# Kernel tuning notes

Hardware: AMD Instinct MI355X
Metric: run time of the kernel (lower is better)

## Reference

```python
import jax, jax.numpy as jnp
import numpy as np

NV, NQ, K, C, FF, H = 40000, 8192, 96, 128, 256, 8
DH = C // H


def _layernorm(x, g, b, eps=1e-5):
    m = jnp.mean(x, axis=-1, keepdims=True)
    v = jnp.var(x, axis=-1, keepdims=True)
    return (x - m) * jax.lax.rsqrt(v + eps) * g + b


def setup_inputs() -> dict:
    key = jax.random.key(0)
    ks = jax.random.split(key, 20)
    voxel_features = jax.random.normal(ks[0], (NV, C), dtype=jnp.float32)
    voxel_coords = jax.random.normal(ks[1], (NV, 3), dtype=jnp.float32)
    query_coords = jax.random.normal(ks[2], (NQ, 3), dtype=jnp.float32)
    raw = jax.random.randint(ks[3], (NQ, K), 0, 50000)
    key_indices = jnp.where(raw >= NV, -1, raw)  # -1 marks padded/missing keys
    key_indices = key_indices.at[:, 0].set(raw[:, 0] % NV)  # ensure >=1 valid key per query
    w = lambda k, shape: (jax.random.normal(k, shape, dtype=jnp.float32) * 0.02)
    return {
        "voxel_features": voxel_features,
        "voxel_coords": voxel_coords,
        "query_coords": query_coords,
        "key_indices": key_indices,
        "norm1_g": jnp.ones((C,), jnp.float32), "norm1_b": jnp.zeros((C,), jnp.float32),
        "q_pos_w": w(ks[4], (C, 3)), "q_pos_b": jnp.zeros((C,), jnp.float32),
        "k_pos_w": w(ks[5], (C, 3)), "k_pos_b": jnp.zeros((C,), jnp.float32),
        "in_w": w(ks[6], (3 * C, C)), "in_b": jnp.zeros((3 * C,), jnp.float32),
        "out_w": w(ks[7], (C, C)), "out_b": jnp.zeros((C,), jnp.float32),
        "norm2_g": jnp.ones((C,), jnp.float32), "norm2_b": jnp.zeros((C,), jnp.float32),
        "lin1_w": w(ks[8], (FF, C)), "lin1_b": jnp.zeros((FF,), jnp.float32),
        "lin2_w": w(ks[9], (C, FF)), "lin2_b": jnp.zeros((C,), jnp.float32),
        "fin_w": w(ks[10], (C, C)), "fin_b": jnp.zeros((C,), jnp.float32),
    }


def reference(voxel_features, voxel_coords, query_coords, key_indices,
              norm1_g, norm1_b, q_pos_w, q_pos_b, k_pos_w, k_pos_b,
              in_w, in_b, out_w, out_b, norm2_g, norm2_b,
              lin1_w, lin1_b, lin2_w, lin2_b, fin_w, fin_b):
    mask = key_indices < 0                      # [NQ, K] True = padded
    idx = jnp.where(mask, 0, key_indices)
    vf = _layernorm(voxel_features, norm1_g, norm1_b)   # norm1
    key_feat = vf[idx]                          # gather: [NQ, K, C]
    key_c = voxel_coords[idx]                   # [NQ, K, 3]
    # q_pos_proj: Linear(3,C)+ReLU ; k_pos_proj: Conv1d(3,C,1)+ReLU (== per-key linear)
    q_feat = jax.nn.relu(query_coords @ q_pos_w.T + q_pos_b)        # [NQ, C]
    key_pos = jax.nn.relu(jnp.einsum('nkt,ct->nkc', key_c, k_pos_w) + k_pos_b)
    key_feat = key_feat + key_pos               # [NQ, K, C]
    # nn.MultiheadAttention: query [1,NQ,C], key/value [K,NQ,C] -> per-query attention over K keys
    wq, wk, wv = in_w[:C], in_w[C:2 * C], in_w[2 * C:]
    bq, bk, bv = in_b[:C], in_b[C:2 * C], in_b[2 * C:]
    q = (q_feat @ wq.T + bq).reshape(NQ, H, DH)                 # [NQ,H,DH]
    k = (key_feat @ wk.T + bk).reshape(NQ, K, H, DH)            # [NQ,K,H,DH]
    v = (key_feat @ wv.T + bv).reshape(NQ, K, H, DH)
    scale = 1.0 / np.sqrt(DH)
    scores = jnp.einsum('nhd,nkhd->nhk', q, k) * scale          # [NQ,H,K]
    scores = jnp.where(mask[:, None, :], jnp.float32(-1e9), scores)
    attn = jax.nn.softmax(scores, axis=-1)
    ctx = jnp.einsum('nhk,nkhd->nhd', attn, v).reshape(NQ, C)
    attend = ctx @ out_w.T + out_b                              # [NQ,C]
    # FFN block (dropout=0 -> identity)
    h = _layernorm(attend, norm2_g, norm2_b)
    act = jax.nn.relu(h @ lin1_w.T + lin1_b) @ lin2_w.T + lin2_b
    x = attend + act
    out = jax.nn.relu(x @ fin_w.T + fin_b)                      # output_layer
    return out
```

## Files before the change

kernel.cpp:

```cpp
#include <hip/hip_runtime.h>
#include <hip/hip_bf16.h>
#include <math.h>

constexpr int NVOX = 40000;
constexpr int NQRY = 8192;
constexpr int KK   = 96;
constexpr int CH   = 128;
constexpr int FFD  = 256;

typedef __attribute__((ext_vector_type(8))) short short8;
typedef __attribute__((ext_vector_type(4))) float float4v;

__device__ inline float bflo(unsigned u) { return __uint_as_float(u << 16); }
__device__ inline float bfhi(unsigned u) { return __uint_as_float(u & 0xffff0000u); }
__device__ inline unsigned short f2bf(float x) {
  union { float f; unsigned u; } a; a.f = x;
  const unsigned r = a.u + 0x7fffu + ((a.u >> 16) & 1u);
  return (unsigned short)(r >> 16);
}
__device__ inline unsigned pack2(float lo, float hi) {
  return (unsigned)f2bf(lo) | ((unsigned)f2bf(hi) << 16);
}

__global__ __launch_bounds__(256) void k_prep(
    const float* __restrict__ vfeat, const float* __restrict__ vcoord,
    const float* __restrict__ n1g, const float* __restrict__ n1b,
    const float* __restrict__ kpw, const float* __restrict__ kpb,
    const float* __restrict__ in_w,
    const float* __restrict__ ow, const float* __restrict__ l1w,
    const float* __restrict__ l2w, const float* __restrict__ fw,
    __hip_bfloat16* __restrict__ Gb, __hip_bfloat16* __restrict__ Wb,
    __hip_bfloat16* __restrict__ Eb) {
  const int b = blockIdx.x;
  const int t = threadIdx.x;
  if (b < NVOX/16) {
    const int vloc = t >> 4;
    const int l    = t & 15;
    const int j = b * 16 + vloc;
    const float4* vrow = reinterpret_cast<const float4*>(vfeat + (size_t)j * CH);
    const float4 x0 = vrow[l*2], x1 = vrow[l*2+1];
    float s  = x0.x+x0.y+x0.z+x0.w + x1.x+x1.y+x1.z+x1.w;
    float ss = x0.x*x0.x+x0.y*x0.y+x0.z*x0.z+x0.w*x0.w
             + x1.x*x1.x+x1.y*x1.y+x1.z*x1.z+x1.w*x1.w;
    #pragma unroll
    for (int m = 8; m >= 1; m >>= 1) { s += __shfl_xor(s, m); ss += __shfl_xor(ss, m); }
    const float mean = s * (1.0f/CH);
    const float var  = ss * (1.0f/CH) - mean*mean;
    const float rstd = 1.0f / sqrtf(var + 1e-5f);
    const float c0 = vcoord[j*3+0], c1 = vcoord[j*3+1], c2 = vcoord[j*3+2];
    const float xv[8] = {x0.x,x0.y,x0.z,x0.w,x1.x,x1.y,x1.z,x1.w};
    float gv[8];
    #pragma unroll
    for (int u = 0; u < 8; u++) {
      const int c = l*8 + u;
      const float vf = (xv[u] - mean) * rstd * n1g[c] + n1b[c];
      const float kp = fmaf(c0, kpw[c*3+0], fmaf(c1, kpw[c*3+1], fmaf(c2, kpw[c*3+2], kpb[c])));
      gv[u] = vf + fmaxf(kp, 0.0f);
    }
    const uint4 pk = make_uint4(pack2(gv[0],gv[1]), pack2(gv[2],gv[3]),
                                pack2(gv[4],gv[5]), pack2(gv[6],gv[7]));
    *reinterpret_cast<uint4*>(Gb + (size_t)j*CH + l*8) = pk;
  } else {
    const int idx = b - NVOX/16;
    const float* src;
    __hip_bfloat16* dst;
    if (idx < 8) {
      const int e = (idx * 256 + t) * 16;
      src = in_w + (size_t)CH*CH + e;
      dst = Wb + e;
    } else {
      const int f = ((idx - 8) * 256 + t) * 16;
      dst = Eb + f;
      if      (f < 16384) src = ow  + f;
      else if (f < 49152) src = l1w + (f - 16384);
      else if (f < 81920) src = l2w + (f - 49152);
      else                src = fw  + (f - 81920);
    }
    float v[16];
    #pragma unroll
    for (int u = 0; u < 4; u++) {
      const float4 fq = *reinterpret_cast<const float4*>(src + u*4);
      v[u*4+0]=fq.x; v[u*4+1]=fq.y; v[u*4+2]=fq.z; v[u*4+3]=fq.w;
    }
    uint4* o = reinterpret_cast<uint4*>(dst);
    o[0] = make_uint4(pack2(v[0],v[1]), pack2(v[2],v[3]),
                      pack2(v[4],v[5]), pack2(v[6],v[7]));
    o[1] = make_uint4(pack2(v[8],v[9]), pack2(v[10],v[11]),
                      pack2(v[12],v[13]), pack2(v[14],v[15]));
  }
}

__global__ __launch_bounds__(256) void k_kv_gemm(
    const __hip_bfloat16* __restrict__ Gb, const __hip_bfloat16* __restrict__ Wb,
    const float* __restrict__ in_b,
    unsigned short* __restrict__ KVh) {
  __shared__ unsigned short ldsD[64][72];
  const int t = threadIdx.x;
  const int w = t >> 6;
  const int lane = t & 63;
  const int col = lane & 15;
  const int quad = lane >> 4;
  const int bx = blockIdx.x;
  const int v0 = (bx >> 2) * 64;
  const int cg = bx & 3;

  const unsigned short* gRow =
      reinterpret_cast<const unsigned short*>(Gb) + (size_t)(v0 + w*16 + col)*CH + quad*8;
  short8 afrag[4];
  #pragma unroll
  for (int kq = 0; kq < 4; kq++)
    afrag[kq] = *reinterpret_cast<const short8*>(gRow + kq*32);

  float4v acc[4];
  #pragma unroll
  for (int j = 0; j < 4; j++) {
    const float bia = in_b[CH + cg*64 + j*16 + col];
    acc[j] = (float4v){bia, bia, bia, bia};
  }
  const unsigned short* wB = reinterpret_cast<const unsigned short*>(Wb);
  #pragma unroll
  for (int kq = 0; kq < 4; kq++) {
    #pragma unroll
    for (int j = 0; j < 4; j++) {
      const short8 bfrag = *reinterpret_cast<const short8*>(
          wB + (size_t)(cg*64 + j*16 + col)*CH + kq*32 + quad*8);
      acc[j] = __builtin_amdgcn_mfma_f32_16x16x32_bf16(afrag[kq], bfrag, acc[j], 0, 0, 0);
    }
  }
  #pragma unroll
  for (int j = 0; j < 4; j++)
    #pragma unroll
    for (int r = 0; r < 4; r++)
      ldsD[w*16 + quad*4 + r][j*16 + col] = f2bf(acc[j][r]);
  __syncthreads();
  const int row = t >> 2;
  const int cc  = (t & 3) * 16;
  const uint4 d0 = *reinterpret_cast<const uint4*>(&ldsD[row][cc]);
  const uint4 d1 = *reinterpret_cast<const uint4*>(&ldsD[row][cc+8]);
  const int head = (cg & 1) * 4 + (cc >> 4);
  const int isV  = cg >> 1;
  unsigned short* dst = KVh + ((size_t)head*NVOX + (v0 + row))*32 + isV*16;
  uint4* out = reinterpret_cast<uint4*>(dst);
  out[0] = d0; out[1] = d1;
}

__global__ __launch_bounds__(256) void k_query(
    const float* __restrict__ qcoord,
    const float* __restrict__ qpw, const float* __restrict__ qpb,
    const float* __restrict__ in_w, const float* __restrict__ in_b,
    float* __restrict__ qout) {
  __shared__ float qf[16][CH];
  const int t = threadIdx.x;
  const int qbase = blockIdx.x * 16;
  #pragma unroll
  for (int i = 0; i < 8; i++) {
    const int e = t + 256*i;
    const int qv = e >> 7, c = e & 127;
    const int qq = qbase + qv;
    const float v = fmaf(qcoord[qq*3+0], qpw[c*3+0],
                    fmaf(qcoord[qq*3+1], qpw[c*3+1],
                    fmaf(qcoord[qq*3+2], qpw[c*3+2], qpb[c])));
    qf[qv][c] = fmaxf(v, 0.0f);
  }
  __syncthreads();
  const int oc = t & 127, half = t >> 7;
  const float* wrow = in_w + (size_t)oc * CH;
  const float bia = in_b[oc];
  float acc[8];
  #pragma unroll
  for (int v = 0; v < 8; v++) acc[v] = bia;
  for (int c = 0; c < CH; c += 4) {
    const float4 w4 = *reinterpret_cast<const float4*>(wrow + c);
    #pragma unroll
    for (int v = 0; v < 8; v++) {
      const float4 g4 = *reinterpret_cast<const float4*>(&qf[half*8+v][c]);
      acc[v] = fmaf(g4.x, w4.x, fmaf(g4.y, w4.y, fmaf(g4.z, w4.z, fmaf(g4.w, w4.w, acc[v]))));
    }
  }
  #pragma unroll
  for (int v = 0; v < 8; v++) qout[(size_t)(qbase + half*8 + v)*CH + oc] = acc[v];
}

__global__ __launch_bounds__(256) void k_attn(
    const unsigned short* __restrict__ KVh,
    const float* __restrict__ qg, const int* __restrict__ kidx,
    float* __restrict__ ctxg) {
  __shared__ float qs[8][16];
  __shared__ float sc[8*104];
  __shared__ float red[128][9];
  __shared__ float rden[8];
  const int t    = threadIdx.x;
  const int h    = blockIdx.x & 7;
  const int n0   = (blockIdx.x >> 3) * 8;
  const int w    = t >> 6;
  const int lane = t & 63;
  const int quad = lane >> 2;
  const int r    = lane & 3;
  const int qh   = quad >> 3;
  const int g    = quad & 7;
  const int q_l  = 2*w + qh;
  const unsigned short* KVbase = KVh + (size_t)h * NVOX * 32;

  if (t < 128) {
    const int q = t >> 4, d = t & 15;
    qs[q][d] = qg[(size_t)(n0 + q)*CH + h*16 + d];
  }
  unsigned msk = 0;
  uint4 kvbuf[12];
  const int krow = (n0 + q_l)*KK + g;
  #pragma unroll
  for (int it = 0; it < 12; it++) {
    const int j0 = kidx[krow + it*8];
    msk |= (unsigned)(j0 < 0) << it;
    const int j = (j0 < 0) ? 0 : j0;
    kvbuf[it] = *reinterpret_cast<const uint4*>(KVbase + (size_t)j*32 + r*8);
  }
  __syncthreads();
  const float4 qa = *reinterpret_cast<const float4*>(&qs[q_l][(r & 1)*8]);
  const float4 qb = *reinterpret_cast<const float4*>(&qs[q_l][(r & 1)*8 + 4]);
  #pragma unroll
  for (int it = 0; it < 12; it++) {
    const uint4 kv = kvbuf[it];
    float s = 0.0f;
    s = fmaf(qa.x, bflo(kv.x), s); s = fmaf(qa.y, bfhi(kv.x), s);
    s = fmaf(qa.z, bflo(kv.y), s); s = fmaf(qa.w, bfhi(kv.y), s);
    s = fmaf(qb.x, bflo(kv.z), s); s = fmaf(qb.y, bfhi(kv.z), s);
    s = fmaf(qb.z, bflo(kv.w), s); s = fmaf(qb.w, bfhi(kv.w), s);
    s += __shfl_xor(s, 1);
    if (r == 0)
      sc[q_l*104 + g + it*8] = ((msk >> it) & 1) ? -1e9f : s * 0.25f;
  }
  __syncthreads();
  if (t < 128) {
    const int q = t >> 4, l = t & 15;
    float mx = -3e38f;
    #pragma unroll
    for (int k = l; k < KK; k += 16) mx = fmaxf(mx, sc[q*104 + k]);
    #pragma unroll
    for (int m = 8; m >= 1; m >>= 1) mx = fmaxf(mx, __shfl_xor(mx, m));
    float sum = 0.0f;
    #pragma unroll
    for (int k = l; k < KK; k += 16) {
      const float p = __expf(sc[q*104 + k] - mx);
      sc[q*104 + k] = p;
      sum += p;
    }
    #pragma unroll
    for (int m = 8; m >= 1; m >>= 1) sum += __shfl_xor(sum, m);
    if (l == 0) rden[q] = 1.0f / sum;
  }
  __syncthreads();
  {
    float acc[8] = {0,0,0,0,0,0,0,0};
    #pragma unroll
    for (int it = 0; it < 12; it++) {
      const float wg = sc[q_l*104 + g + it*8];
      const uint4 kv = kvbuf[it];
      acc[0] = fmaf(wg, bflo(kv.x), acc[0]); acc[1] = fmaf(wg, bfhi(kv.x), acc[1]);
      acc[2] = fmaf(wg, bflo(kv.y), acc[2]); acc[3] = fmaf(wg, bfhi(kv.y), acc[3]);
      acc[4] = fmaf(wg, bflo(kv.z), acc[4]); acc[5] = fmaf(wg, bfhi(kv.z), acc[5]);
      acc[6] = fmaf(wg, bflo(kv.w), acc[6]); acc[7] = fmaf(wg, bfhi(kv.w), acc[7]);
    }
    if (r >= 2) {
      const int slot = q_l*16 + g*2 + (r - 2);
      #pragma unroll
      for (int u = 0; u < 8; u++) red[slot][u] = acc[u];
    }
  }
  __syncthreads();
  if (t < 128) {
    const int q = t >> 4, d = t & 15;
    const int half = d >> 3, u = d & 7;
    float s = 0.0f;
    #pragma unroll
    for (int gg = 0; gg < 8; gg++) s += red[q*16 + gg*2 + half][u];
    ctxg[(size_t)(n0 + q)*CH + h*16 + d] = s * rden[q];
  }
}

__global__ __launch_bounds__(256) void k_epi(
    const float* __restrict__ ctxg, const __hip_bfloat16* __restrict__ Eb,
    const float* __restrict__ ob,
    const float* __restrict__ n2g, const float* __restrict__ n2b,
    const float* __restrict__ l1b, const float* __restrict__ l2b,
    const float* __restrict__ fb,
    float* __restrict__ outp) {
  __shared__ unsigned short csb[16][136];
  __shared__ float attnS[16][132];
  __shared__ unsigned short hb[16][136];
  __shared__ unsigned short a1b[16][264];
  __shared__ unsigned short xb[16][136];
  const unsigned short* owb  = reinterpret_cast<const unsigned short*>(Eb);
  const unsigned short* l1wb = owb + 16384;
  const unsigned short* l2wb = owb + 49152;
  const unsigned short* fwb  = owb + 81920;

  const int t = threadIdx.x;
  const int w = t >> 6;
  const int lane = t & 63;
  const int col = lane & 15;
  const int quad = lane >> 4;
  const int qbase = blockIdx.x * 16;

  {
    const int e = t * 8;
    const int row = e >> 7, cc = e & 127;
    const float4* src = reinterpret_cast<const float4*>(ctxg + (size_t)(qbase+row)*CH + cc);
    const float4 x0 = src[0], x1 = src[1];
    *reinterpret_cast<uint4*>(&csb[row][cc]) =
        make_uint4(pack2(x0.x,x0.y), pack2(x0.z,x0.w), pack2(x1.x,x1.y), pack2(x1.z,x1.w));
  }
  __syncthreads();
  {
    short8 af[4];
    #pragma unroll
    for (int kq = 0; kq < 4; kq++)
      af[kq] = *reinterpret_cast<const short8*>(&csb[col][quad*8 + kq*32]);
    #pragma unroll
    for (int j = 0; j < 2; j++) {
      const int n0 = w*32 + j*16;
      const float bia = ob[n0 + col];
      float4v acc = (float4v){bia, bia, bia, bia};
      #pragma unroll
      for (int kq = 0; kq < 4; kq++) {
        const short8 bf = *reinterpret_cast<const short8*>(
            owb + (size_t)(n0 + col)*CH + kq*32 + quad*8);
        acc = __builtin_amdgcn_mfma_f32_16x16x32_bf16(af[kq], bf, acc, 0, 0, 0);
      }
      #pragma unroll
      for (int r = 0; r < 4; r++) attnS[quad*4 + r][n0 + col] = acc[r];
    }
  }
  __syncthreads();
  {
    const int row = t >> 4, l = t & 15;
    float s = 0.0f, ss = 0.0f;
    #pragma unroll
    for (int c = l; c < CH; c += 16) { const float x = attnS[row][c]; s += x; ss += x*x; }
    #pragma unroll
    for (int m = 8; m >= 1; m >>= 1) { s += __shfl_xor(s, m); ss += __shfl_xor(ss, m); }
    const float mean = s * (1.0f/CH);
    const float var  = ss * (1.0f/CH) - mean*mean;
    const float rstd = 1.0f / sqrtf(var + 1e-5f);
    #pragma unroll
    for (int c = l; c < CH; c += 16)
      hb[row][c] = f2bf((attnS[row][c] - mean) * rstd * n2g[c] + n2b[c]);
  }
  __syncthreads();
  {
    short8 af[4];
    #pragma unroll
    for (int kq = 0; kq < 4; kq++)
      af[kq] = *reinterpret_cast<const short8*>(&hb[col][quad*8 + kq*32]);
    #pragma unroll
    for (int j = 0; j < 4; j++) {
      const int n0 = w*64 + j*16;
      const float bia = l1b[n0 + col];
      float4v acc = (float4v){bia, bia, bia, bia};
      #pragma unroll
      for (int kq = 0; kq < 4; kq++) {
        const short8 bf = *reinterpret_cast<const short8*>(
            l1wb + (size_t)(n0 + col)*CH + kq*32 + quad*8);
        acc = __builtin_amdgcn_mfma_f32_16x16x32_bf16(af[kq], bf, acc, 0, 0, 0);
      }
      #pragma unroll
      for (int r = 0; r < 4; r++)
        a1b[quad*4 + r][n0 + col] = f2bf(fmaxf(acc[r], 0.0f));
    }
  }
  __syncthreads();
  {
    short8 af[8];
    #pragma unroll
    for (int kq = 0; kq < 8; kq++)
      af[kq] = *reinterpret_cast<const short8*>(&a1b[col][quad*8 + kq*32]);
    #pragma unroll
    for (int j = 0; j < 2; j++) {
      const int n0 = w*32 + j*16;
      const float bia = l2b[n0 + col];
      float4v acc = (float4v){bia, bia, bia, bia};
      #pragma unroll
      for (int kq = 0; kq < 8; kq++) {
        const short8 bf = *reinterpret_cast<const short8*>(
            l2wb + (size_t)(n0 + col)*FFD + kq*32 + quad*8);
        acc = __builtin_amdgcn_mfma_f32_16x16x32_bf16(af[kq], bf, acc, 0, 0, 0);
      }
      #pragma unroll
      for (int r = 0; r < 4; r++)
        xb[quad*4 + r][n0 + col] = f2bf(acc[r] + attnS[quad*4 + r][n0 + col]);
    }
  }
  __syncthreads();
  {
    short8 af[4];
    #pragma unroll
    for (int kq = 0; kq < 4; kq++)
      af[kq] = *reinterpret_cast<const short8*>(&xb[col][quad*8 + kq*32]);
    #pragma unroll
    for (int j = 0; j < 2; j++) {
      const int n0 = w*32 + j*16;
      const float bia = fb[n0 + col];
      float4v acc = (float4v){bia, bia, bia, bia};
      #pragma unroll
      for (int kq = 0; kq < 4; kq++) {
        const short8 bf = *reinterpret_cast<const short8*>(
            fwb + (size_t)(n0 + col)*CH + kq*32 + quad*8);
        acc = __builtin_amdgcn_mfma_f32_16x16x32_bf16(af[kq], bf, acc, 0, 0, 0);
      }
      #pragma unroll
      for (int r = 0; r < 4; r++)
        outp[(size_t)(qbase + quad*4 + r)*CH + n0 + col] = fmaxf(acc[r], 0.0f);
    }
  }
}

extern "C" void kernel_launch(void* const* d_in, const int* in_sizes, int n_in,
                              void* d_out, int out_size, void* d_ws, size_t ws_size,
                              hipStream_t stream) {
  const float* vfeat  = (const float*)d_in[0];
  const float* vcoord = (const float*)d_in[1];
  const float* qcoord = (const float*)d_in[2];
  const int*   kidx   = (const int*)  d_in[3];
  const float* n1g    = (const float*)d_in[4];
  const float* n1b    = (const float*)d_in[5];
  const float* qpw    = (const float*)d_in[6];
  const float* qpb    = (const float*)d_in[7];
  const float* kpw    = (const float*)d_in[8];
  const float* kpb    = (const float*)d_in[9];
  const float* in_w   = (const float*)d_in[10];
  const float* in_b   = (const float*)d_in[11];
  const float* out_w  = (const float*)d_in[12];
  const float* out_b  = (const float*)d_in[13];
  const float* n2g    = (const float*)d_in[14];
  const float* n2b    = (const float*)d_in[15];
  const float* l1w    = (const float*)d_in[16];
  const float* l1b    = (const float*)d_in[17];
  const float* l2w    = (const float*)d_in[18];
  const float* l2b    = (const float*)d_in[19];
  const float* fw     = (const float*)d_in[20];
  const float* fb     = (const float*)d_in[21];
  float* out = (float*)d_out;

  unsigned short* KVh = (unsigned short*)d_ws;
  __hip_bfloat16* Gb = (__hip_bfloat16*)(KVh + (size_t)8*NVOX*32);
  __hip_bfloat16* Wb = Gb + (size_t)NVOX*CH;
  __hip_bfloat16* Eb = Wb + (size_t)2*CH*CH;
  float* qb = (float*)(Eb + 98304);
  float* cx = qb + (size_t)NQRY*CH;

  k_prep   <<<NVOX/16 + 32, 256, 0, stream>>>(vfeat, vcoord, n1g, n1b, kpw, kpb,
                                              in_w, out_w, l1w, l2w, fw, Gb, Wb, Eb);
  k_query  <<<NQRY/16, 256, 0, stream>>>(qcoord, qpw, qpb, in_w, in_b, qb);
  k_kv_gemm<<<(NVOX/64)*4, 256, 0, stream>>>(Gb, Wb, in_b, KVh);
  k_attn   <<<(NQRY/8)*8, 256, 0, stream>>>(KVh, qb, kidx, cx);
  k_epi    <<<NQRY/16, 256, 0, stream>>>(cx, Eb, out_b, n2g, n2b, l1b, l2b, fb, out);
}
```

Baseline: 209.6 us.

## Fold query projection into prep kernel and make attention softmax register-resident

The query projection kernel becomes extra blocks of the prep kernel, which removes one launch and lets the two independent jobs share the GPU. The attention kernel now keeps scores in registers. Softmax max and sum are done with cross-lane shuffles, and the context reduction uses shuffles too, replacing shared-memory staging and four block-wide barriers. The cost is more shuffle traffic and a larger per-thread register array, and the prep kernel's shared-memory footprint grows for all of its blocks.

New measurement: 216.7 us. +3.4%, slower.

```diff
diff --git a/kernel.cpp b/kernel.cpp
--- a/kernel.cpp
+++ b/kernel.cpp
@@ -26,11 +26,13 @@
     const float* __restrict__ vfeat, const float* __restrict__ vcoord,
     const float* __restrict__ n1g, const float* __restrict__ n1b,
     const float* __restrict__ kpw, const float* __restrict__ kpb,
-    const float* __restrict__ in_w,
+    const float* __restrict__ in_w, const float* __restrict__ in_b,
     const float* __restrict__ ow, const float* __restrict__ l1w,
     const float* __restrict__ l2w, const float* __restrict__ fw,
+    const float* __restrict__ qcoord,
+    const float* __restrict__ qpw, const float* __restrict__ qpb,
     __hip_bfloat16* __restrict__ Gb, __hip_bfloat16* __restrict__ Wb,
-    __hip_bfloat16* __restrict__ Eb) {
+    __hip_bfloat16* __restrict__ Eb, float* __restrict__ qout) {
   const int b = blockIdx.x;
   const int t = threadIdx.x;
   if (b < NVOX/16) {
@@ -60,7 +62,7 @@
     const uint4 pk = make_uint4(pack2(gv[0],gv[1]), pack2(gv[2],gv[3]),
                                 pack2(gv[4],gv[5]), pack2(gv[6],gv[7]));
     *reinterpret_cast<uint4*>(Gb + (size_t)j*CH + l*8) = pk;
-  } else {
+  } else if (b < NVOX/16 + 32) {
     const int idx = b - NVOX/16;
     const float* src;
     __hip_bfloat16* dst;
@@ -87,6 +89,36 @@
                       pack2(v[4],v[5]), pack2(v[6],v[7]));
     o[1] = make_uint4(pack2(v[8],v[9]), pack2(v[10],v[11]),
                       pack2(v[12],v[13]), pack2(v[14],v[15]));
+  } else {
+    __shared__ float qf[16][CH];
+    const int qbase = (b - (NVOX/16 + 32)) * 16;
+    #pragma unroll
+    for (int i = 0; i < 8; i++) {
+      const int e = t + 256*i;
+      const int qv = e >> 7, c = e & 127;
+      const int qq = qbase + qv;
+      const float v = fmaf(qcoord[qq*3+0], qpw[c*3+0],
+                      fmaf(qcoord[qq*3+1], qpw[c*3+1],
+                      fmaf(qcoord[qq*3+2], qpw[c*3+2], qpb[c])));
+      qf[qv][c] = fmaxf(v, 0.0f);
+    }
+    __syncthreads();
+    const int oc = t & 127, half = t >> 7;
+    const float* wrow = in_w + (size_t)oc * CH;
+    const float bia = in_b[oc];
+    float acc[8];
+    #pragma unroll
+    for (int v = 0; v < 8; v++) acc[v] = bia;
+    for (int c = 0; c < CH; c += 4) {
+      const float4 w4 = *reinterpret_cast<const float4*>(wrow + c);
+      #pragma unroll
+      for (int v = 0; v < 8; v++) {
+        const float4 g4 = *reinterpret_cast<const float4*>(&qf[half*8+v][c]);
+        acc[v] = fmaf(g4.x, w4.x, fmaf(g4.y, w4.y, fmaf(g4.z, w4.z, fmaf(g4.w, w4.w, acc[v]))));
+      }
+    }
+    #pragma unroll
+    for (int v = 0; v < 8; v++) qout[(size_t)(qbase + half*8 + v)*CH + oc] = acc[v];
   }
 }
 
@@ -144,70 +176,28 @@
   out[0] = d0; out[1] = d1;
 }
 
-__global__ __launch_bounds__(256) void k_query(
-    const float* __restrict__ qcoord,
-    const float* __restrict__ qpw, const float* __restrict__ qpb,
-    const float* __restrict__ in_w, const float* __restrict__ in_b,
-    float* __restrict__ qout) {
-  __shared__ float qf[16][CH];
-  const int t = threadIdx.x;
-  const int qbase = blockIdx.x * 16;
-  #pragma unroll
-  for (int i = 0; i < 8; i++) {
-    const int e = t + 256*i;
-    const int qv = e >> 7, c = e & 127;
-    const int qq = qbase + qv;
-    const float v = fmaf(qcoord[qq*3+0], qpw[c*3+0],
-                    fmaf(qcoord[qq*3+1], qpw[c*3+1],
-                    fmaf(qcoord[qq*3+2], qpw[c*3+2], qpb[c])));
-    qf[qv][c] = fmaxf(v, 0.0f);
-  }
-  __syncthreads();
-  const int oc = t & 127, half = t >> 7;
-  const float* wrow = in_w + (size_t)oc * CH;
-  const float bia = in_b[oc];
-  float acc[8];
-  #pragma unroll
-  for (int v = 0; v < 8; v++) acc[v] = bia;
-  for (int c = 0; c < CH; c += 4) {
-    const float4 w4 = *reinterpret_cast<const float4*>(wrow + c);
-    #pragma unroll
-    for (int v = 0; v < 8; v++) {
-      const float4 g4 = *reinterpret_cast<const float4*>(&qf[half*8+v][c]);
-      acc[v] = fmaf(g4.x, w4.x, fmaf(g4.y, w4.y, fmaf(g4.z, w4.z, fmaf(g4.w, w4.w, acc[v]))));
-    }
-  }
-  #pragma unroll
-  for (int v = 0; v < 8; v++) qout[(size_t)(qbase + half*8 + v)*CH + oc] = acc[v];
-}
-
 __global__ __launch_bounds__(256) void k_attn(
     const unsigned short* __restrict__ KVh,
     const float* __restrict__ qg, const int* __restrict__ kidx,
     float* __restrict__ ctxg) {
-  __shared__ float qs[8][16];
-  __shared__ float sc[8*104];
-  __shared__ float red[128][9];
-  __shared__ float rden[8];
   const int t    = threadIdx.x;
   const int h    = blockIdx.x & 7;
   const int n0   = (blockIdx.x >> 3) * 8;
   const int w    = t >> 6;
   const int lane = t & 63;
-  const int quad = lane >> 2;
+  const int qh   = lane >> 5;
+  const int g    = (lane >> 2) & 7;
   const int r    = lane & 3;
-  const int qh   = quad >> 3;
-  const int g    = quad & 7;
-  const int q_l  = 2*w + qh;
+  const int q    = n0 + 2*w + qh;
   const unsigned short* KVbase = KVh + (size_t)h * NVOX * 32;
 
-  if (t < 128) {
-    const int q = t >> 4, d = t & 15;
-    qs[q][d] = qg[(size_t)(n0 + q)*CH + h*16 + d];
-  }
+  const float* qrow = qg + (size_t)q*CH + h*16 + (r & 1)*8;
+  const float4 qa = *reinterpret_cast<const float4*>(qrow);
+  const float4 qb = *reinterpret_cast<const float4*>(qrow + 4);
+
   unsigned msk = 0;
   uint4 kvbuf[12];
-  const int krow = (n0 + q_l)*KK + g;
+  const int krow = q*KK + g;
   #pragma unroll
   for (int it = 0; it < 12; it++) {
     const int j0 = kidx[krow + it*8];
@@ -215,9 +205,7 @@
     const int j = (j0 < 0) ? 0 : j0;
     kvbuf[it] = *reinterpret_cast<const uint4*>(KVbase + (size_t)j*32 + r*8);
   }
-  __syncthreads();
-  const float4 qa = *reinterpret_cast<const float4*>(&qs[q_l][(r & 1)*8]);
-  const float4 qb = *reinterpret_cast<const float4*>(&qs[q_l][(r & 1)*8 + 4]);
+  float sv[12];
   #pragma unroll
   for (int it = 0; it < 12; it++) {
     const uint4 kv = kvbuf[it];
@@ -227,54 +215,44 @@
     s = fmaf(qb.x, bflo(kv.z), s); s = fmaf(qb.y, bfhi(kv.z), s);
     s = fmaf(qb.z, bflo(kv.w), s); s = fmaf(qb.w, bfhi(kv.w), s);
     s += __shfl_xor(s, 1);
-    if (r == 0)
-      sc[q_l*104 + g + it*8] = ((msk >> it) & 1) ? -1e9f : s * 0.25f;
-  }
-  __syncthreads();
-  if (t < 128) {
-    const int q = t >> 4, l = t & 15;
-    float mx = -3e38f;
-    #pragma unroll
-    for (int k = l; k < KK; k += 16) mx = fmaxf(mx, sc[q*104 + k]);
-    #pragma unroll
-    for (int m = 8; m >= 1; m >>= 1) mx = fmaxf(mx, __shfl_xor(mx, m));
-    float sum = 0.0f;
-    #pragma unroll
-    for (int k = l; k < KK; k += 16) {
-      const float p = __expf(sc[q*104 + k] - mx);
-      sc[q*104 + k] = p;
-      sum += p;
-    }
-    #pragma unroll
-    for (int m = 8; m >= 1; m >>= 1) sum += __shfl_xor(sum, m);
-    if (l == 0) rden[q] = 1.0f / sum;
-  }
-  __syncthreads();
-  {
-    float acc[8] = {0,0,0,0,0,0,0,0};
-    #pragma unroll
-    for (int it = 0; it < 12; it++) {
-      const float wg = sc[q_l*104 + g + it*8];
-      const uint4 kv = kvbuf[it];
-      acc[0] = fmaf(wg, bflo(kv.x), acc[0]); acc[1] = fmaf(wg, bfhi(kv.x), acc[1]);
-      acc[2] = fmaf(wg, bflo(kv.y), acc[2]); acc[3] = fmaf(wg, bfhi(kv.y), acc[3]);
-      acc[4] = fmaf(wg, bflo(kv.z), acc[4]); acc[5] = fmaf(wg, bfhi(kv.z), acc[5]);
-      acc[6] = fmaf(wg, bflo(kv.w), acc[6]); acc[7] = fmaf(wg, bfhi(kv.w), acc[7]);
-    }
-    if (r >= 2) {
-      const int slot = q_l*16 + g*2 + (r - 2);
-      #pragma unroll
-      for (int u = 0; u < 8; u++) red[slot][u] = acc[u];
-    }
-  }
-  __syncthreads();
-  if (t < 128) {
-    const int q = t >> 4, d = t & 15;
-    const int half = d >> 3, u = d & 7;
-    float s = 0.0f;
-    #pragma unroll
-    for (int gg = 0; gg < 8; gg++) s += red[q*16 + gg*2 + half][u];
-    ctxg[(size_t)(n0 + q)*CH + h*16 + d] = s * rden[q];
+    sv[it] = ((msk >> it) & 1) ? -1e9f : s * 0.25f;
+  }
+  float mx = sv[0];
+  #pragma unroll
+  for (int it = 1; it < 12; it++) mx = fmaxf(mx, sv[it]);
+  mx = fmaxf(mx, __shfl_xor(mx, 4));
+  mx = fmaxf(mx, __shfl_xor(mx, 8));
+  mx = fmaxf(mx, __shfl_xor(mx, 16));
+  float sum = 0.0f;
+  #pragma unroll
+  for (int it = 0; it < 12; it++) { sv[it] = __expf(sv[it] - mx); sum += sv[it]; }
+  sum += __shfl_xor(sum, 4);
+  sum += __shfl_xor(sum, 8);
+  sum += __shfl_xor(sum, 16);
+  const float inv = 1.0f / sum;
+  const int qlane = lane & ~3;
+  #pragma unroll
+  for (int it = 0; it < 12; it++) sv[it] = __shfl(sv[it] * inv, qlane);
+  float acc[8] = {0,0,0,0,0,0,0,0};
+  #pragma unroll
+  for (int it = 0; it < 12; it++) {
+    const float wg = sv[it];
+    const uint4 kv = kvbuf[it];
+    acc[0] = fmaf(wg, bflo(kv.x), acc[0]); acc[1] = fmaf(wg, bfhi(kv.x), acc[1]);
+    acc[2] = fmaf(wg, bflo(kv.y), acc[2]); acc[3] = fmaf(wg, bfhi(kv.y), acc[3]);
+    acc[4] = fmaf(wg, bflo(kv.z), acc[4]); acc[5] = fmaf(wg, bfhi(kv.z), acc[5]);
+    acc[6] = fmaf(wg, bflo(kv.w), acc[6]); acc[7] = fmaf(wg, bfhi(kv.w), acc[7]);
+  }
+  #pragma unroll
+  for (int u = 0; u < 8; u++) {
+    acc[u] += __shfl_xor(acc[u], 4);
+    acc[u] += __shfl_xor(acc[u], 8);
+    acc[u] += __shfl_xor(acc[u], 16);
+  }
+  if (r >= 2 && g == 0) {
+    float* dst = ctxg + (size_t)q*CH + h*16 + (r - 2)*8;
+    *reinterpret_cast<float4*>(dst)     = make_float4(acc[0], acc[1], acc[2], acc[3]);
+    *reinterpret_cast<float4*>(dst + 4) = make_float4(acc[4], acc[5], acc[6], acc[7]);
   }
 }
 
@@ -448,9 +426,9 @@
   float* qb = (float*)(Eb + 98304);
   float* cx = qb + (size_t)NQRY*CH;
 
-  k_prep   <<<NVOX/16 + 32, 256, 0, stream>>>(vfeat, vcoord, n1g, n1b, kpw, kpb,
-                                              in_w, out_w, l1w, l2w, fw, Gb, Wb, Eb);
-  k_query  <<<NQRY/16, 256, 0, stream>>>(qcoord, qpw, qpb, in_w, in_b, qb);
+  k_prep   <<<NVOX/16 + 32 + NQRY/16, 256, 0, stream>>>(
+      vfeat, vcoord, n1g, n1b, kpw, kpb, in_w, in_b,
+      out_w, l1w, l2w, fw, qcoord, qpw, qpb, Gb, Wb, Eb, qb);
   k_kv_gemm<<<(NVOX/64)*4, 256, 0, stream>>>(Gb, Wb, in_b, KVh);
   k_attn   <<<(NQRY/8)*8, 256, 0, stream>>>(KVh, qb, kidx, cx);
   k_epi    <<<NQRY/16, 256, 0, stream>>>(cx, Eb, out_b, n2g, n2b, l1b, l2b, fb, out);
```

## Fold query projection into prep kernel and add cache-warming pass before attention

Applied to the files above, without the earlier changes.

Merges the query projection kernel into the prep kernel as extra blocks, saving one launch and letting that work overlap voxel normalization. Adds a k_warm kernel that reads the whole K/V table, the key indices and the query buffer right before attention, aiming to leave them in the last-level cache so the attention gathers hit in cache. The warm pass adds an extra full read of these buffers and one more launch, which only pays off if they stay resident in cache.

Result: no change. 211.2 us (+0.8%).

```diff
diff --git a/kernel.cpp b/kernel.cpp
--- a/kernel.cpp
+++ b/kernel.cpp
@@ -26,11 +26,13 @@
     const float* __restrict__ vfeat, const float* __restrict__ vcoord,
     const float* __restrict__ n1g, const float* __restrict__ n1b,
     const float* __restrict__ kpw, const float* __restrict__ kpb,
-    const float* __restrict__ in_w,
+    const float* __restrict__ in_w, const float* __restrict__ in_b,
     const float* __restrict__ ow, const float* __restrict__ l1w,
     const float* __restrict__ l2w, const float* __restrict__ fw,
+    const float* __restrict__ qcoord,
+    const float* __restrict__ qpw, const float* __restrict__ qpb,
     __hip_bfloat16* __restrict__ Gb, __hip_bfloat16* __restrict__ Wb,
-    __hip_bfloat16* __restrict__ Eb) {
+    __hip_bfloat16* __restrict__ Eb, float* __restrict__ qout) {
   const int b = blockIdx.x;
   const int t = threadIdx.x;
   if (b < NVOX/16) {
@@ -60,7 +62,7 @@
     const uint4 pk = make_uint4(pack2(gv[0],gv[1]), pack2(gv[2],gv[3]),
                                 pack2(gv[4],gv[5]), pack2(gv[6],gv[7]));
     *reinterpret_cast<uint4*>(Gb + (size_t)j*CH + l*8) = pk;
-  } else {
+  } else if (b < NVOX/16 + 32) {
     const int idx = b - NVOX/16;
     const float* src;
     __hip_bfloat16* dst;
@@ -87,6 +89,36 @@
                       pack2(v[4],v[5]), pack2(v[6],v[7]));
     o[1] = make_uint4(pack2(v[8],v[9]), pack2(v[10],v[11]),
                       pack2(v[12],v[13]), pack2(v[14],v[15]));
+  } else {
+    __shared__ float qf[16][CH];
+    const int qbase = (b - (NVOX/16 + 32)) * 16;
+    #pragma unroll
+    for (int i = 0; i < 8; i++) {
+      const int e = t + 256*i;
+      const int qv = e >> 7, c = e & 127;
+      const int qq = qbase + qv;
+      const float v = fmaf(qcoord[qq*3+0], qpw[c*3+0],
+                      fmaf(qcoord[qq*3+1], qpw[c*3+1],
+                      fmaf(qcoord[qq*3+2], qpw[c*3+2], qpb[c])));
+      qf[qv][c] = fmaxf(v, 0.0f);
+    }
+    __syncthreads();
+    const int oc = t & 127, half = t >> 7;
+    const float* wrow = in_w + (size_t)oc * CH;
+    const float bia = in_b[oc];
+    float acc[8];
+    #pragma unroll
+    for (int v = 0; v < 8; v++) acc[v] = bia;
+    for (int c = 0; c < CH; c += 4) {
+      const float4 w4 = *reinterpret_cast<const float4*>(wrow + c);
+      #pragma unroll
+      for (int v = 0; v < 8; v++) {
+        const float4 g4 = *reinterpret_cast<const float4*>(&qf[half*8+v][c]);
+        acc[v] = fmaf(g4.x, w4.x, fmaf(g4.y, w4.y, fmaf(g4.z, w4.z, fmaf(g4.w, w4.w, acc[v]))));
+      }
+    }
+    #pragma unroll
+    for (int v = 0; v < 8; v++) qout[(size_t)(qbase + half*8 + v)*CH + oc] = acc[v];
   }
 }
 
@@ -144,41 +176,30 @@
   out[0] = d0; out[1] = d1;
 }
 
-__global__ __launch_bounds__(256) void k_query(
-    const float* __restrict__ qcoord,
-    const float* __restrict__ qpw, const float* __restrict__ qpb,
-    const float* __restrict__ in_w, const float* __restrict__ in_b,
-    float* __restrict__ qout) {
-  __shared__ float qf[16][CH];
+__global__ __launch_bounds__(256) void k_warm(
+    const uint4* __restrict__ kv4, const uint4* __restrict__ kidx4,
+    const uint4* __restrict__ qg4, unsigned* __restrict__ sink) {
+  const int b = blockIdx.x;
   const int t = threadIdx.x;
-  const int qbase = blockIdx.x * 16;
-  #pragma unroll
-  for (int i = 0; i < 8; i++) {
-    const int e = t + 256*i;
-    const int qv = e >> 7, c = e & 127;
-    const int qq = qbase + qv;
-    const float v = fmaf(qcoord[qq*3+0], qpw[c*3+0],
-                    fmaf(qcoord[qq*3+1], qpw[c*3+1],
-                    fmaf(qcoord[qq*3+2], qpw[c*3+2], qpb[c])));
-    qf[qv][c] = fmaxf(v, 0.0f);
-  }
-  __syncthreads();
-  const int oc = t & 127, half = t >> 7;
-  const float* wrow = in_w + (size_t)oc * CH;
-  const float bia = in_b[oc];
-  float acc[8];
-  #pragma unroll
-  for (int v = 0; v < 8; v++) acc[v] = bia;
-  for (int c = 0; c < CH; c += 4) {
-    const float4 w4 = *reinterpret_cast<const float4*>(wrow + c);
-    #pragma unroll
-    for (int v = 0; v < 8; v++) {
-      const float4 g4 = *reinterpret_cast<const float4*>(&qf[half*8+v][c]);
-      acc[v] = fmaf(g4.x, w4.x, fmaf(g4.y, w4.y, fmaf(g4.z, w4.z, fmaf(g4.w, w4.w, acc[v]))));
-    }
-  }
-  #pragma unroll
-  for (int v = 0; v < 8; v++) qout[(size_t)(qbase + half*8 + v)*CH + oc] = acc[v];
+  unsigned acc = 0;
+  if (b < 1000) {
+    const int h = b & 7, chunk = b >> 3;
+    const uint4* p = kv4 + (size_t)h*160000 + (size_t)chunk*1280 + t;
+    #pragma unroll
+    for (int i = 0; i < 5; i++) {
+      const uint4 v = p[i*256];
+      acc ^= v.x ^ v.y ^ v.z ^ v.w;
+    }
+  } else {
+    const int off = (b - 1000) * 4096 + t;
+    #pragma unroll
+    for (int i = 0; i < 16; i++) {
+      const int idx = off + i*256;
+      const uint4 v = (idx < 196608) ? kidx4[idx] : qg4[idx - 196608];
+      acc ^= v.x ^ v.y ^ v.z ^ v.w;
+    }
+  }
+  if (acc == 0xDEADBEEFu) sink[0] = acc;
 }
 
 __global__ __launch_bounds__(256) void k_attn(
@@ -447,11 +468,14 @@
   __hip_bfloat16* Eb = Wb + (size_t)2*CH*CH;
   float* qb = (float*)(Eb + 98304);
   float* cx = qb + (size_t)NQRY*CH;
-
-  k_prep   <<<NVOX/16 + 32, 256, 0, stream>>>(vfeat, vcoord, n1g, n1b, kpw, kpb,
-                                              in_w, out_w, l1w, l2w, fw, Gb, Wb, Eb);
-  k_query  <<<NQRY/16, 256, 0, stream>>>(qcoord, qpw, qpb, in_w, in_b, qb);
+  unsigned* sink = (unsigned*)(cx + (size_t)NQRY*CH);
+
+  k_prep   <<<NVOX/16 + 32 + NQRY/16, 256, 0, stream>>>(
+      vfeat, vcoord, n1g, n1b, kpw, kpb, in_w, in_b,
+      out_w, l1w, l2w, fw, qcoord, qpw, qpb, Gb, Wb, Eb, qb);
   k_kv_gemm<<<(NVOX/64)*4, 256, 0, stream>>>(Gb, Wb, in_b, KVh);
+  k_warm   <<<1112, 256, 0, stream>>>((const uint4*)KVh, (const uint4*)kidx,
+                                      (const uint4*)qb, sink);
   k_attn   <<<(NQRY/8)*8, 256, 0, stream>>>(KVh, qb, kidx, cx);
   k_epi    <<<NQRY/16, 256, 0, stream>>>(cx, Eb, out_b, n2g, n2b, l1b, l2b, fb, out);
 }
```
